# Kernel optimization log

Hardware: AMD Instinct MI355X
Metric: run time of the kernel (lower is better)

## Reference

```python
import jax, jax.numpy as jnp
import numpy as np

NG = 8       # GroupNorm groups
EPS = 1e-5   # torch default eps for GroupNorm/BatchNorm
M_AND = 5    # Anderson history size
MAX_ITER = 25
LAM = 1e-4
BETA = 1.0


def conv2d(x, w):
    # x: [B,C,H,W], w: [O,I,3,3], stride 1, SAME padding (pad=1)
    return jax.lax.conv_general_dilated(x, w, (1, 1), 'SAME',
                                        dimension_numbers=('NCHW', 'OIHW', 'NCHW'))


def group_norm(x, g, b):
    B, C, H, W = x.shape
    xg = x.reshape(B, NG, C // NG, H, W)
    mu = xg.mean((2, 3, 4), keepdims=True)
    var = xg.var((2, 3, 4), keepdims=True)
    xn = ((xg - mu) * jax.lax.rsqrt(var + EPS)).reshape(B, C, H, W)
    return xn * g[None, :, None, None] + b[None, :, None, None]


def batch_norm(x, g, b):
    # training-mode BatchNorm2d: batch statistics over (B,H,W)
    mu = x.mean((0, 2, 3), keepdims=True)
    var = x.var((0, 2, 3), keepdims=True)
    return (x - mu) * jax.lax.rsqrt(var + EPS) * g[None, :, None, None] + b[None, :, None, None]


def resnet_f(p, z, x):
    # y = norm1(relu(conv1(z))); out = norm3(relu(z + norm2(x + conv2(y))))
    y = group_norm(jax.nn.relu(conv2d(z, p['conv1_w'])), p['gn1_g'], p['gn1_b'])
    return group_norm(jax.nn.relu(z + group_norm(x + conv2d(y, p['conv2_w']),
                                                 p['gn2_g'], p['gn2_b'])),
                      p['gn3_g'], p['gn3_b'])


def anderson(f, x0, m=M_AND, lam=LAM, max_iter=MAX_ITER, beta=BETA):
    # Anderson acceleration for fixed point z = f(z); fixed iteration count
    # (the torch version early-exits at tol=0.01; we run the full max_iter for
    # a deterministic jit-friendly reference).
    shape = x0.shape
    bsz = shape[0]
    flat = lambda v: v.reshape(bsz, -1)
    X = [None] * m
    Fv = [None] * m
    X[0] = flat(x0)
    Fv[0] = flat(f(x0))
    X[1] = Fv[0]
    Fv[1] = flat(f(Fv[0].reshape(shape)))
    for k in range(2, max_iter):
        n = min(k, m)
        Xn = jnp.stack(X[:n], 1)   # [B,n,D]
        Fn = jnp.stack(Fv[:n], 1)  # [B,n,D]
        G = Fn - Xn
        Hm = jnp.einsum('bnd,bmd->bnm', G, G) + lam * jnp.eye(n, dtype=x0.dtype)
        Hb = (jnp.zeros((bsz, n + 1, n + 1), x0.dtype)
              .at[:, 1:, 1:].set(Hm)
              .at[:, 0, 1:].set(1.0)
              .at[:, 1:, 0].set(1.0))
        y = jnp.zeros((bsz, n + 1), x0.dtype).at[:, 0].set(1.0)
        alpha = jnp.linalg.solve(Hb, y[..., None])[:, 1:, 0]  # [B,n]
        xk = beta * jnp.einsum('bn,bnd->bd', alpha, Fn) + (1.0 - beta) * jnp.einsum('bn,bnd->bd', alpha, Xn)
        X[k % m] = xk
        Fv[k % m] = flat(f(xk.reshape(shape)))
    return X[(max_iter - 1) % m].reshape(shape)


def setup_inputs() -> dict:
    key = jax.random.key(0)
    ks = jax.random.split(key, 6)
    B, H, W = 8, 128, 200
    f32 = jnp.float32
    return {
        'x': jax.random.normal(ks[0], (B, 1, H, W), f32),
        'conv0_w': jax.random.normal(ks[1], (48, 1, 3, 3), f32) * 0.1,
        'conv0_b': jnp.zeros((48,), f32),
        'bn_g': jnp.ones((48,), f32),
        'bn_b': jnp.zeros((48,), f32),
        'conv1_w': jax.random.normal(ks[2], (64, 48, 3, 3), f32) * 0.01,
        'conv2_w': jax.random.normal(ks[3], (48, 64, 3, 3), f32) * 0.01,
        'gn1_g': jnp.ones((64,), f32), 'gn1_b': jnp.zeros((64,), f32),
        'gn2_g': jnp.ones((48,), f32), 'gn2_b': jnp.zeros((48,), f32),
        'gn3_g': jnp.ones((48,), f32), 'gn3_b': jnp.zeros((48,), f32),
        'fc_w': jax.random.normal(ks[4], (10, 200), f32) * 0.05,
        'fc_b': jnp.zeros((10,), f32),
    }


def reference(x, conv0_w, conv0_b, bn_g, bn_b, conv1_w, conv2_w,
              gn1_g, gn1_b, gn2_g, gn2_b, gn3_g, gn3_b, fc_w, fc_b):
    fp = {'conv1_w': conv1_w, 'conv2_w': conv2_w,
          'gn1_g': gn1_g, 'gn1_b': gn1_b,
          'gn2_g': gn2_g, 'gn2_b': gn2_b,
          'gn3_g': gn3_g, 'gn3_b': gn3_b}
    h = batch_norm(conv2d(x, conv0_w) + conv0_b[None, :, None, None], bn_g, bn_b)
    z_star = anderson(lambda z: resnet_f(fp, z, h), jnp.zeros_like(h))
    z = resnet_f(fp, z_star, h)  # one extra application, as in DEQFixedPoint
    # Linear(200,10) acts on last dim: [B,48,H,200] -> [B,48,H,10]
    return jnp.einsum('bchw,ow->bcho', z, fc_w) + fc_b
```

## Files before the change

### kernel.cpp

```cpp
#include <hip/hip_runtime.h>

#define BB   8
#define HH   128
#define WW   200
#define HWSZ 25600
#define C48  48
#define C64  64
#define NGRP 8
#define EPSV 1e-5f
#define LAMV 1e-4
#define SLOT 9830400
#define DPB  1228800
#define Y64SZ 13107200
#define BIGELEMS 131072000ull

typedef unsigned short bf16_t;
typedef __attribute__((ext_vector_type(4))) short s4v;
typedef __attribute__((ext_vector_type(8))) short s8v;
typedef __attribute__((ext_vector_type(16))) float f32x16;

__device__ inline float b2f(bf16_t b) { return __uint_as_float(((unsigned)b) << 16); }
__device__ inline bf16_t f2b(float f) {
    unsigned u = __float_as_uint(f);
    unsigned r = u + 0x7fffu + ((u >> 16) & 1u);
    return (bf16_t)(r >> 16);
}
__device__ inline float lo16(unsigned u) { return __uint_as_float(u << 16); }
__device__ inline float hi16(unsigned u) { return __uint_as_float(u & 0xffff0000u); }
__device__ inline unsigned pack2(float lo, float hi) {
    return ((unsigned)f2b(lo)) | (((unsigned)f2b(hi)) << 16);
}
__device__ inline float4 ld4(const bf16_t* p) {
    ushort4 u = *(const ushort4*)p;
    return make_float4(b2f(u.x), b2f(u.y), b2f(u.z), b2f(u.w));
}
__device__ inline void st4(bf16_t* p, float4 v) {
    ushort4 u; u.x = f2b(v.x); u.y = f2b(v.y); u.z = f2b(v.z); u.w = f2b(v.w);
    *(ushort4*)p = u;
}
__device__ inline void ld8(const bf16_t* p, float* v) {
    uint4 u = *(const uint4*)p;
    v[0] = lo16(u.x); v[1] = hi16(u.x); v[2] = lo16(u.y); v[3] = hi16(u.y);
    v[4] = lo16(u.z); v[5] = hi16(u.z); v[6] = lo16(u.w); v[7] = hi16(u.w);
}
__device__ inline void st8(bf16_t* p, const float* v) {
    uint4 u;
    u.x = pack2(v[0], v[1]); u.y = pack2(v[2], v[3]);
    u.z = pack2(v[4], v[5]); u.w = pack2(v[6], v[7]);
    *(uint4*)p = u;
}

__device__ inline void ms_from(const double* __restrict__ ds, int pair, double invcnt,
                               float& mean, float& inv) {
    double s = ds[2 * pair], q = ds[2 * pair + 1];
    double m = s * invcnt;
    double v = q * invcnt - m * m;
    mean = (float)m;
    inv = (float)(1.0 / sqrt(v + (double)EPSV));
}


__global__ void zero_kernel(float* __restrict__ p, int n) {
    int i = blockIdx.x * 256 + threadIdx.x;
    if (i < n) p[i] = 0.f;
}
__global__ void fill16_kernel(float4* __restrict__ p) {
    float4 z; z.x = z.y = z.z = z.w = 0.f;
    p[(size_t)blockIdx.x * 256 + threadIdx.x] = z;
}
__global__ void copy16_kernel(float4* __restrict__ dst, const float4* __restrict__ src) {
    size_t i = (size_t)blockIdx.x * 256 + threadIdx.x;
    dst[i] = src[i];
}

__global__ void pack_kernel(const float* __restrict__ w, bf16_t* __restrict__ apk,
                            int CIN, int CO_real, int total) {
    int idx = blockIdx.x * 256 + threadIdx.x;
    if (idx >= total) return;
    int j   = idx & 7;
    int l   = (idx >> 3) & 63;
    int mt  = (idx >> 9) & 1;
    int tap = (idx >> 10) % 9;
    int kc  = idx / 9216;
    int co = mt * 32 + (l & 31);
    int ci = kc * 16 + (l >> 5) * 8 + j;
    float v = (co < CO_real) ? w[((size_t)co * CIN + ci) * 9 + tap] : 0.f;
    apk[idx] = f2b(v);
}

__global__ __launch_bounds__(256) void conv0_kernel(
    const float* __restrict__ x, const float* __restrict__ w0,
    const float* __restrict__ b0, float* __restrict__ out)
{
    __shared__ float xs[3 * 202];
    __shared__ float wt[480];
    const int tid = threadIdx.x;
    const int bI = blockIdx.x / HH, y = blockIdx.x % HH;
    for (int i = tid; i < 606; i += 256) {
        int r = i / 202, cc = i % 202;
        int gy = y + r - 1, gx = cc - 1;
        float v = 0.f;
        if ((unsigned)gy < (unsigned)HH && (unsigned)gx < (unsigned)WW)
            v = x[(size_t)bI * HWSZ + gy * WW + gx];
        xs[r * 202 + cc] = v;
    }
    for (int i = tid; i < 480; i += 256) wt[i] = (i < 432) ? w0[i] : b0[i - 432];
    __syncthreads();
    const size_t obase = (((size_t)bI * HH + y) * WW) * 48;
    for (int ch = tid; ch < 2400; ch += 256) {
        int px = (ch * 4) / 48, c0 = (ch * 4) % 48;
        float xv[3][3];
        #pragma unroll
        for (int r = 0; r < 3; r++)
            #pragma unroll
            for (int dx = 0; dx < 3; dx++)
                xv[r][dx] = xs[r * 202 + px + dx];
        float4 o;
        #pragma unroll
        for (int j = 0; j < 4; j++) {
            int c = c0 + j;
            float acc = wt[432 + c];
            #pragma unroll
            for (int r = 0; r < 3; r++)
                #pragma unroll
                for (int dx = 0; dx < 3; dx++)
                    acc = fmaf(xv[r][dx], wt[c * 9 + r * 3 + dx], acc);
            ((float*)&o)[j] = acc;
        }
        *(float4*)(out + obase + ch * 4) = o;
    }
}

__global__ void bn_stats_kernel(const float* __restrict__ src, double* __restrict__ dst)
{
    __shared__ float ss[192], qq[192];
    const int tid = threadIdx.x;
    const int c = tid % 48, r = tid / 48;
    const int b = blockIdx.y;
    const size_t base = ((size_t)b * HWSZ + (size_t)blockIdx.x * 256) * 48 + c;
    float s = 0.f, q = 0.f;
    for (int p = r; p < 256; p += 4) {
        float v = src[base + (size_t)p * 48];
        s += v; q += v * v;
    }
    ss[tid] = s; qq[tid] = q;
    __syncthreads();
    if (tid < 48) {
        s = ss[tid] + ss[tid + 48] + ss[tid + 96] + ss[tid + 144];
        q = qq[tid] + qq[tid + 48] + qq[tid + 96] + qq[tid + 144];
        unsafeAtomicAdd(&dst[tid * 2],     (double)s);
        unsafeAtomicAdd(&dst[tid * 2 + 1], (double)q);
    }
}

__global__ __launch_bounds__(256) void bn_apply_kernel(
    const float* __restrict__ src, bf16_t* __restrict__ dst,
    const float* __restrict__ gamma, const float* __restrict__ beta,
    const double* __restrict__ ds)
{
    __shared__ float gaT[48], beT[48];
    int tid = threadIdx.x;
    if (tid < 48) {
        float mean, inv; ms_from(ds, tid, 1.0 / 204800.0, mean, inv);
        float ga = gamma[tid] * inv;
        gaT[tid] = ga; beT[tid] = beta[tid] - mean * ga;
    }
    __syncthreads();
    size_t base = (size_t)blockIdx.x * 1024 + (size_t)tid * 4;
    int c0 = (int)(base % 48);
    float4 v = *(const float4*)(src + base);
    ushort4 o;
    o.x = f2b(fmaf(v.x, gaT[c0],     beT[c0]));
    o.y = f2b(fmaf(v.y, gaT[c0 + 1], beT[c0 + 1]));
    o.z = f2b(fmaf(v.z, gaT[c0 + 2], beT[c0 + 2]));
    o.w = f2b(fmaf(v.w, gaT[c0 + 3], beT[c0 + 3]));
    *(ushort4*)(dst + base) = o;
}

template<int CIN, int CIPAD, int CO, int OTS, int CG, bool RELU, bool ADDH, bool FOLDGN>
__global__ __launch_bounds__(512) void conv_mfma_kernel(
    const bf16_t* __restrict__ in, const s8v* __restrict__ apk,
    const bf16_t* __restrict__ hadd, bf16_t* __restrict__ out,
    double* __restrict__ dsOut,
    const double* __restrict__ dsPrev, const float* __restrict__ gPrev,
    const float* __restrict__ bPrev)
{
    constexpr int KC  = CIN / 16;
    constexpr int NCH = CIN / 4;
    const int tid  = threadIdx.x;
    const int lane = tid & 63;
    const int wv   = tid >> 6;
    const int x0 = blockIdx.x * 32;
    const int y0 = blockIdx.y * 8;
    const int b  = blockIdx.z;

    __shared__ __align__(16) bf16_t bt[10 * 34 * CIPAD];
    __shared__ __align__(16) float gaT[FOLDGN ? CIN : 4];
    __shared__ __align__(16) float beT[FOLDGN ? CIN : 4];
    __shared__ float ss[512], qq[512];

    if (FOLDGN) {
        if (tid < CIN) {
            float mean, inv;
            ms_from(dsPrev, b * NGRP + tid / (CIN / NGRP), 1.0 / 204800.0, mean, inv);
            float ga = gPrev[tid] * inv;
            gaT[tid] = ga; beT[tid] = bPrev[tid] - mean * ga;
        }
        __syncthreads();
    }
    for (int i = tid; i < 10 * 34 * NCH; i += 512) {
        int ch = i % NCH, p = i / NCH;
        int r = p / 34, c = p - r * 34;
        int gy = y0 + r - 1, gx = x0 + c - 1;
        ushort4 v = make_ushort4(0, 0, 0, 0);
        if ((unsigned)gy < (unsigned)HH && (unsigned)gx < (unsigned)WW) {
            ushort4 raw = *(const ushort4*)(in + ((((size_t)b * HH + gy) * WW + gx) * CIN + ch * 4));
            if (FOLDGN) {
                float4 ga4 = *(const float4*)&gaT[ch * 4];
                float4 be4 = *(const float4*)&beT[ch * 4];
                v.x = f2b(fmaf(b2f(raw.x), ga4.x, be4.x));
                v.y = f2b(fmaf(b2f(raw.y), ga4.y, be4.y));
                v.z = f2b(fmaf(b2f(raw.z), ga4.z, be4.z));
                v.w = f2b(fmaf(b2f(raw.w), ga4.w, be4.w));
            } else v = raw;
        }
        *(ushort4*)(bt + p * CIPAD + ch * 4) = v;
    }
    __syncthreads();

    const int n = lane & 31, half = lane >> 5;
    f32x16 acc0, acc1;
    #pragma unroll
    for (int i = 0; i < 16; i++) { acc0[i] = 0.f; acc1[i] = 0.f; }

    #pragma unroll
    for (int ky = 0; ky < 3; ky++)
    #pragma unroll
    for (int kx = 0; kx < 3; kx++) {
        const int tap = ky * 3 + kx;
        s8v af[2 * KC];
        #pragma unroll
        for (int kc = 0; kc < KC; kc++) {
            af[2 * kc]     = apk[(size_t)kc * 1152 + tap * 128 + lane];
            af[2 * kc + 1] = apk[(size_t)kc * 1152 + tap * 128 + 64 + lane];
        }
        const bf16_t* brow = bt + ((wv + ky) * 34 + n + kx) * CIPAD + half * 8;
        #pragma unroll
        for (int kc = 0; kc < KC; kc++) {
            s8v bfrag = *(const s8v*)(brow + kc * 16);
            acc0 = __builtin_amdgcn_mfma_f32_32x32x16_bf16(af[2 * kc],     bfrag, acc0, 0, 0, 0);
            acc1 = __builtin_amdgcn_mfma_f32_32x32x16_bf16(af[2 * kc + 1], bfrag, acc1, 0, 0, 0);
        }
    }
    __syncthreads();

    bf16_t* ot = bt;
    {
        const int pxl = wv * 32 + n;
        const bool pv = (x0 + n) < WW;
        #pragma unroll
        for (int g4 = 0; g4 < 4; g4++) {
            s4v pk0;
            #pragma unroll
            for (int jj = 0; jj < 4; jj++) {
                float v = acc0[g4 * 4 + jj];
                if (RELU) v = fmaxf(v, 0.f);
                pk0[jj] = (short)(pv ? f2b(v) : (bf16_t)0);
            }
            *(s4v*)&ot[pxl * OTS + g4 * 8 + 4 * half] = pk0;
            const int c1b = 32 + g4 * 8 + 4 * half;
            if (c1b + 3 < CO) {
                s4v pk1;
                #pragma unroll
                for (int jj = 0; jj < 4; jj++) {
                    float v = acc1[g4 * 4 + jj];
                    if (RELU) v = fmaxf(v, 0.f);
                    pk1[jj] = (short)(pv ? f2b(v) : (bf16_t)0);
                }
                *(s4v*)&ot[pxl * OTS + c1b] = pk1;
            }
        }
    }
    __syncthreads();
    {
        constexpr int NCH8 = 256 * CO / 8;
        for (int ch = tid; ch < NCH8; ch += 512) {
            int pxl = ch / (CO / 8);
            int co0 = (ch % (CO / 8)) * 8;
            int row = pxl >> 5, col = pxl & 31;
            int xx = x0 + col;
            if (xx < WW) {
                bf16_t* lp = &ot[pxl * OTS + co0];
                size_t ga = (((size_t)b * HH + y0 + row) * WW + xx) * CO + co0;
                if (ADDH) {
                    float4 h0 = ld4(hadd + ga), h1 = ld4(hadd + ga + 4);
                    float4 l0 = ld4(lp), l1 = ld4(lp + 4);
                    float4 v0 = make_float4(l0.x + h0.x, l0.y + h0.y, l0.z + h0.z, l0.w + h0.w);
                    float4 v1 = make_float4(l1.x + h1.x, l1.y + h1.y, l1.z + h1.z, l1.w + h1.w);
                    st4(out + ga, v0); st4(out + ga + 4, v1);
                    st4(lp, v0); st4(lp + 4, v1);
                } else {
                    *(ushort4*)(out + ga)     = *(ushort4*)lp;
                    *(ushort4*)(out + ga + 4) = *(ushort4*)(lp + 4);
                }
            }
        }
    }
    if (ADDH) __syncthreads();
    {
        constexpr int NPH = 512 / CO;
        const int c = tid % CO, rr = tid / CO;
        float s = 0.f, q = 0.f;
        if (rr < NPH) {
            for (int px = rr; px < 256; px += NPH) {
                float v = b2f(ot[px * OTS + c]);
                s += v; q += v * v;
            }
        }
        ss[tid] = s; qq[tid] = q;
        __syncthreads();
        if (tid < CO) {
            float S = ss[tid], Q = qq[tid];
            #pragma unroll
            for (int p = 1; p < NPH; p++) { S += ss[tid + p * CO]; Q += qq[tid + p * CO]; }
            ss[tid] = S; qq[tid] = Q;
        }
        __syncthreads();
        if (tid < NGRP) {
            float S = 0.f, Q = 0.f;
            #pragma unroll
            for (int j = 0; j < CG; j++) { S += ss[tid * CG + j]; Q += qq[tid * CG + j]; }
            unsafeAtomicAdd(&dsOut[((size_t)b * NGRP + tid) * 2],     (double)S);
            unsafeAtomicAdd(&dsOut[((size_t)b * NGRP + tid) * 2 + 1], (double)Q);
        }
    }
}

__global__ __launch_bounds__(192) void add_relu_gn2_kernel(
    bf16_t* __restrict__ u, const bf16_t* __restrict__ z,
    const double* __restrict__ ds2, const float* __restrict__ g2,
    const float* __restrict__ b2, double* __restrict__ ds3)
{
    __shared__ float sm[16];
    const int tid = threadIdx.x;
    const int c0 = 8 * (tid % 6), pxr = tid / 6;
    const int b = blockIdx.y;
    if (tid < 16) sm[tid] = 0.f;
    const int gA = c0 / 6;
    const int split = (gA + 1) * 6 - c0;
    float meanA, invA, meanB, invB;
    ms_from(ds2, b * NGRP + gA,     1.0 / 153600.0, meanA, invA);
    ms_from(ds2, b * NGRP + gA + 1, 1.0 / 153600.0, meanB, invB);
    float wga[8], wbe[8];
    #pragma unroll
    for (int e = 0; e < 8; e++) {
        int c = c0 + e;
        float m = (e < split) ? meanA : meanB, iv = (e < split) ? invA : invB;
        float ga = g2[c] * iv;
        wga[e] = ga; wbe[e] = b2[c] - m * ga;
    }
    __syncthreads();
    const size_t pxbase = (size_t)b * HWSZ + (size_t)blockIdx.x * 256;
    float sA = 0.f, qA = 0.f, sB = 0.f, qB = 0.f;
    for (int it = 0; it < 8; it++) {
        size_t idx = (pxbase + it * 32 + pxr) * 48 + c0;
        float uu[8], zz[8], vv[8];
        ld8(u + idx, uu); ld8(z + idx, zz);
        #pragma unroll
        for (int e = 0; e < 8; e++) {
            float v = fmaxf(fmaf(uu[e], wga[e], wbe[e]) + zz[e], 0.f);
            vv[e] = v;
            if (e < split) { sA += v; qA += v * v; } else { sB += v; qB += v * v; }
        }
        st8(u + idx, vv);
    }
    atomicAdd(&sm[2 * gA], sA);     atomicAdd(&sm[2 * gA + 1], qA);
    atomicAdd(&sm[2 * gA + 2], sB); atomicAdd(&sm[2 * gA + 3], qB);
    __syncthreads();
    if (tid < NGRP) {
        unsafeAtomicAdd(&ds3[(b * NGRP + tid) * 2],     (double)sm[tid * 2]);
        unsafeAtomicAdd(&ds3[(b * NGRP + tid) * 2 + 1], (double)sm[tid * 2 + 1]);
    }
}

__global__ __launch_bounds__(192) void gn3_gram_kernel(
    const bf16_t* __restrict__ v, const bf16_t* __restrict__ z,
    bf16_t* __restrict__ F, bf16_t* __restrict__ G,
    const double* __restrict__ ds3, const float* __restrict__ g3,
    const float* __restrict__ b3,
    const bf16_t* __restrict__ Gall, int jslot, int nf, double* __restrict__ gram)
{
    __shared__ double red[3][5];
    const int tid = threadIdx.x;
    const int c0 = 8 * (tid % 6), pxr = tid / 6;
    const int b = blockIdx.y;
    const int gA = c0 / 6;
    const int split = (gA + 1) * 6 - c0;
    float meanA, invA, meanB, invB;
    ms_from(ds3, b * NGRP + gA,     1.0 / 153600.0, meanA, invA);
    ms_from(ds3, b * NGRP + gA + 1, 1.0 / 153600.0, meanB, invB);
    float wga[8], wbe[8];
    #pragma unroll
    for (int e = 0; e < 8; e++) {
        int c = c0 + e;
        float m = (e < split) ? meanA : meanB, iv = (e < split) ? invA : invB;
        float ga = g3[c] * iv;
        wga[e] = ga; wbe[e] = b3[c] - m * ga;
    }
    const size_t pxbase = (size_t)b * HWSZ + (size_t)blockIdx.x * 256;
    double dot[5] = {0.0, 0.0, 0.0, 0.0, 0.0};
    for (int it = 0; it < 8; it++) {
        size_t idx = (pxbase + it * 32 + pxr) * 48 + c0;
        float rr[8];
        ld8(v + idx, rr);
        #pragma unroll
        for (int e = 0; e < 8; e++) rr[e] = fmaf(rr[e], wga[e], wbe[e]);
        st8(F + idx, rr);
        if (nf > 0) {
            float zz[8], gg[8];
            ld8(z + idx, zz);
            #pragma unroll
            for (int e = 0; e < 8; e++) gg[e] = rr[e] - zz[e];
            st8(G + idx, gg);
            #pragma unroll
            for (int i = 0; i < 5; i++) {
                if (i >= nf) continue;
                float d = 0.f;
                if (i == jslot) {
                    #pragma unroll
                    for (int e = 0; e < 8; e++) d = fmaf(gg[e], gg[e], d);
                } else {
                    float gi[8];
                    ld8(Gall + (size_t)i * SLOT + idx, gi);
                    #pragma unroll
                    for (int e = 0; e < 8; e++) d = fmaf(gg[e], gi[e], d);
                }
                dot[i] += (double)d;
            }
        }
    }
    if (nf > 0) {
        #pragma unroll
        for (int i = 0; i < 5; i++) {
            if (i >= nf) continue;
            #pragma unroll
            for (int off = 32; off > 0; off >>= 1) dot[i] += __shfl_down(dot[i], off);
        }
        int wv = tid >> 6;
        if ((tid & 63) == 0) {
            #pragma unroll
            for (int i = 0; i < 5; i++) if (i < nf) red[wv][i] = dot[i];
        }
        __syncthreads();
        if (tid == 0) {
            #pragma unroll
            for (int i = 0; i < 5; i++) {
                if (i >= nf) continue;
                double D = red[0][i] + red[1][i] + red[2][i];
                unsafeAtomicAdd(&gram[b * 25 + jslot * 5 + i], D);
                if (i != jslot) unsafeAtomicAdd(&gram[b * 25 + i * 5 + jslot], D);
            }
        }
    }
}


__global__ void solve_kernel(const double* __restrict__ gram, float* __restrict__ alpha, int n) {
    int b = threadIdx.x;
    if (b >= BB) return;
    const int m = n + 1;
    double A[6][7];
    for (int i = 0; i < m; i++)
        for (int jj = 0; jj <= m; jj++) A[i][jj] = 0.0;
    for (int i = 1; i < m; i++) { A[0][i] = 1.0; A[i][0] = 1.0; }
    for (int i = 1; i < m; i++)
        for (int jj = 1; jj < m; jj++)
            A[i][jj] = gram[b * 25 + (i - 1) * 5 + (jj - 1)] + ((i == jj) ? LAMV : 0.0);
    A[0][m] = 1.0;
    for (int col = 0; col < m; col++) {
        int piv = col; double best = fabs(A[col][col]);
        for (int rr = col + 1; rr < m; rr++) {
            double tv = fabs(A[rr][col]);
            if (tv > best) { best = tv; piv = rr; }
        }
        if (piv != col)
            for (int cc = col; cc <= m; cc++) {
                double tmp = A[col][cc]; A[col][cc] = A[piv][cc]; A[piv][cc] = tmp;
            }
        double invp = 1.0 / A[col][col];
        for (int cc = col; cc <= m; cc++) A[col][cc] *= invp;
        for (int rr = 0; rr < m; rr++) {
            if (rr == col) continue;
            double f = A[rr][col];
            if (f != 0.0)
                for (int cc = col; cc <= m; cc++) A[rr][cc] = fma(-f, A[col][cc], A[rr][cc]);
        }
    }
    for (int i = 0; i < n; i++) alpha[b * 5 + i] = (float)A[i + 1][m];
}

__global__ __launch_bounds__(256) void xk_kernel(
    const bf16_t* __restrict__ Fb, const float* __restrict__ alpha,
    bf16_t* __restrict__ zcur, int n, double* __restrict__ gram, int jz, int nf)
{
    if (blockIdx.x == 0 && threadIdx.x < 8 * nf) {
        int b = threadIdx.x / nf, i = threadIdx.x % nf;
        gram[b * 25 + jz * 5 + i] = 0.0;
        gram[b * 25 + i * 5 + jz] = 0.0;
    }
    const int b = blockIdx.x / 75;
    float al[5];
    #pragma unroll
    for (int j = 0; j < 5; j++) al[j] = (j < n) ? alpha[b * 5 + j] : 0.f;
    const size_t base = (size_t)blockIdx.x * 16384 + (size_t)threadIdx.x * 8;
    for (int it = 0; it < 8; it++) {
        size_t idx = base + (size_t)it * 2048;
        float s[8] = {0.f, 0.f, 0.f, 0.f, 0.f, 0.f, 0.f, 0.f};
        #pragma unroll
        for (int j = 0; j < 5; j++) {
            if (j < n) {
                float f[8];
                ld8(Fb + (size_t)j * SLOT + idx, f);
                #pragma unroll
                for (int e = 0; e < 8; e++) s[e] = fmaf(f[e], al[j], s[e]);
            }
        }
        st8(zcur + idx, s);
    }
}

__global__ __launch_bounds__(512) void fc_kernel(
    const bf16_t* __restrict__ zf, const float* __restrict__ fw,
    const float* __restrict__ fb, float* __restrict__ out)
{
    __shared__ bf16_t row[9600];
    __shared__ float fwT[2000];
    int tid = threadIdx.x;
    int b = blockIdx.x >> 7, hh = blockIdx.x & 127;
    size_t base = (((size_t)b * HH + hh) * WW) * 48;
    for (int i = tid; i < 2400; i += 512)
        *(ushort4*)&row[i * 4] = *(const ushort4*)(zf + base + (size_t)i * 4);
    for (int i = tid; i < 2000; i += 512) fwT[i] = fw[i];
    __syncthreads();
    if (tid < 480) {
        int c = tid % 48, o = tid / 48;
        float acc = fb[o];
        #pragma unroll 4
        for (int w = 0; w < 200; w++)
            acc = fmaf(b2f(row[w * 48 + c]), fwT[o * 200 + w], acc);
        out[(((size_t)b * 48 + c) * HH + hh) * 10 + o] = acc;
    }
}


static inline int imin(int a, int b) { return a < b ? a : b; }

extern "C" void kernel_launch(void* const* d_in, const int* in_sizes, int n_in,
                              void* d_out, int out_size, void* d_ws, size_t ws_size,
                              hipStream_t stream)
{
    const float* x   = (const float*)d_in[0];
    const float* w0  = (const float*)d_in[1];
    const float* b0  = (const float*)d_in[2];
    const float* bng = (const float*)d_in[3];
    const float* bnb = (const float*)d_in[4];
    const float* w1  = (const float*)d_in[5];
    const float* w2  = (const float*)d_in[6];
    const float* g1  = (const float*)d_in[7];
    const float* be1 = (const float*)d_in[8];
    const float* g2  = (const float*)d_in[9];
    const float* be2 = (const float*)d_in[10];
    const float* g3  = (const float*)d_in[11];
    const float* be3 = (const float*)d_in[12];
    const float* fcw = (const float*)d_in[13];
    const float* fcb = (const float*)d_in[14];
    float* out = (float*)d_out;

    bf16_t* h    = (bf16_t*)d_ws;
    bf16_t* zcur = h + (size_t)SLOT;
    bf16_t* y64  = zcur + (size_t)SLOT;
    bf16_t* Fb   = y64 + (size_t)Y64SZ;
    bf16_t* Gb   = Fb + 5 * (size_t)SLOT;
    double* dstats = (double*)((char*)d_ws + BIGELEMS * 2);
    double* gram   = dstats + 9696;
    float*  alpha  = (float*)(gram + 200);
    bf16_t* apk1   = (bf16_t*)(alpha + 40);
    bf16_t* apk2   = apk1 + 27648;
    float*  scratch = (float*)Gb;

    const size_t need = BIGELEMS * 2 + 9696 * 8 + 200 * 8 + 40 * 4 + (27648 + 36864) * 2;
    if (ws_size < need) return;

    const dim3 blk(256);
    const int CHUNKS16 = SLOT * 2 / 16 / 256;

    zero_kernel<<<(19792 + 255) / 256, blk, 0, stream>>>((float*)dstats, 19792);
    pack_kernel<<<108, blk, 0, stream>>>(w1, apk1, 48, 64, 27648);
    pack_kernel<<<144, blk, 0, stream>>>(w2, apk2, 64, 48, 36864);
    fill16_kernel<<<CHUNKS16, blk, 0, stream>>>((float4*)zcur);

    conv0_kernel<<<BB * HH, blk, 0, stream>>>(x, w0, b0, scratch);
    bn_stats_kernel<<<dim3(100, BB), dim3(192), 0, stream>>>(scratch, dstats);
    bn_apply_kernel<<<SLOT / 1024, blk, 0, stream>>>(scratch, h, bng, bnb, dstats);

    int call = 0;
    auto resnet = [&](const bf16_t* zin, bf16_t* Fdst, bf16_t* Gdst, int jslot, int nf) {
        double* ds = dstats + 96 + 384 * call;
        call++;
        dim3 cg(7, 16, BB);
        conv_mfma_kernel<48, 56, 64, 66, 8, true, false, false><<<cg, dim3(512), 0, stream>>>(
            zin, (const s8v*)apk1, nullptr, y64, ds, nullptr, nullptr, nullptr);
        conv_mfma_kernel<64, 72, 48, 50, 6, false, true, true><<<cg, dim3(512), 0, stream>>>(
            y64, (const s8v*)apk2, h, Fdst, ds + 128, ds, g1, be1);
        add_relu_gn2_kernel<<<dim3(100, BB), dim3(192), 0, stream>>>(
            Fdst, zin, ds + 128, g2, be2, ds + 256);
        gn3_gram_kernel<<<dim3(100, BB), dim3(192), 0, stream>>>(
            Fdst, zin, Fdst, Gdst, ds + 256, g3, be3, Gb, jslot, nf, gram);
    };

    resnet(zcur, Fb, Gb, 0, 1);
    copy16_kernel<<<CHUNKS16, blk, 0, stream>>>((float4*)zcur, (const float4*)Fb);
    resnet(zcur, Fb + (size_t)SLOT, Gb + (size_t)SLOT, 1, 2);

    for (int k = 2; k <= 24; k++) {
        int n = imin(k, 5);
        int j = k % 5;
        int nf = imin(k + 1, 5);
        solve_kernel<<<1, 64, 0, stream>>>(gram, alpha, n);
        xk_kernel<<<600, blk, 0, stream>>>(Fb, alpha, zcur, n, gram, j, nf);
        if (k < 24)
            resnet(zcur, Fb + (size_t)j * SLOT, Gb + (size_t)j * SLOT, j, nf);
    }

    resnet(zcur, Fb, nullptr, 0, 0);

    fc_kernel<<<BB * HH, dim3(512), 0, stream>>>(Fb, fcw, fcb, out);
}
```

Measured before the change: 4.970 ms.

## Shrink conv tiles, double-buffer weight loads, fuse Anderson solve into xk

The MFMA conv kernel moves from 512-thread blocks over 8 rows to 256-thread blocks over 4 rows with launch bounds (256,4). This aims for more resident blocks per CU and finer-grained scheduling, at the cost of more halo reloads. Weight fragment loads are now double-buffered across taps so global loads overlap the MFMAs. The separate solve kernel is dropped: each xk block redundantly solves the small Anderson system in one thread, and the gram zeroing moves into add_relu_gn2, removing one launch per iteration.

```diff
diff --git a/kernel.cpp b/kernel.cpp
--- a/kernel.cpp
+++ b/kernel.cpp
@@ -178,7 +178,7 @@
 }
 
 template<int CIN, int CIPAD, int CO, int OTS, int CG, bool RELU, bool ADDH, bool FOLDGN>
-__global__ __launch_bounds__(512) void conv_mfma_kernel(
+__global__ __launch_bounds__(256, 4) void conv_mfma_kernel(
     const bf16_t* __restrict__ in, const s8v* __restrict__ apk,
     const bf16_t* __restrict__ hadd, bf16_t* __restrict__ out,
     double* __restrict__ dsOut,
@@ -191,13 +191,13 @@
     const int lane = tid & 63;
     const int wv   = tid >> 6;
     const int x0 = blockIdx.x * 32;
-    const int y0 = blockIdx.y * 8;
+    const int y0 = blockIdx.y * 4;
     const int b  = blockIdx.z;
 
-    __shared__ __align__(16) bf16_t bt[10 * 34 * CIPAD];
+    __shared__ __align__(16) bf16_t bt[6 * 34 * CIPAD];
     __shared__ __align__(16) float gaT[FOLDGN ? CIN : 4];
     __shared__ __align__(16) float beT[FOLDGN ? CIN : 4];
-    __shared__ float ss[512], qq[512];
+    __shared__ float ss[256], qq[256];
 
     if (FOLDGN) {
         if (tid < CIN) {
@@ -208,7 +208,7 @@
         }
         __syncthreads();
     }
-    for (int i = tid; i < 10 * 34 * NCH; i += 512) {
+    for (int i = tid; i < 6 * 34 * NCH; i += 256) {
         int ch = i % NCH, p = i / NCH;
         int r = p / 34, c = p - r * 34;
         int gy = y0 + r - 1, gx = x0 + c - 1;
@@ -233,25 +233,36 @@
     #pragma unroll
     for (int i = 0; i < 16; i++) { acc0[i] = 0.f; acc1[i] = 0.f; }
 
-    #pragma unroll
-    for (int ky = 0; ky < 3; ky++)
-    #pragma unroll
-    for (int kx = 0; kx < 3; kx++) {
-        const int tap = ky * 3 + kx;
-        s8v af[2 * KC];
+    const s8v* apw = apk + lane;
+    s8v afA[2 * KC], afB[2 * KC];
+
+    auto ld_tap = [&](int tap, s8v* dst) {
         #pragma unroll
         for (int kc = 0; kc < KC; kc++) {
-            af[2 * kc]     = apk[(size_t)kc * 1152 + tap * 128 + lane];
-            af[2 * kc + 1] = apk[(size_t)kc * 1152 + tap * 128 + 64 + lane];
-        }
+            dst[2 * kc]     = apw[(size_t)kc * 1152 + tap * 128];
+            dst[2 * kc + 1] = apw[(size_t)kc * 1152 + tap * 128 + 64];
+        }
+    };
+    auto do_tap = [&](int tap, const s8v* cur) {
+        const int ky = tap / 3, kx = tap % 3;
         const bf16_t* brow = bt + ((wv + ky) * 34 + n + kx) * CIPAD + half * 8;
         #pragma unroll
         for (int kc = 0; kc < KC; kc++) {
             s8v bfrag = *(const s8v*)(brow + kc * 16);
-            acc0 = __builtin_amdgcn_mfma_f32_32x32x16_bf16(af[2 * kc],     bfrag, acc0, 0, 0, 0);
-            acc1 = __builtin_amdgcn_mfma_f32_32x32x16_bf16(af[2 * kc + 1], bfrag, acc1, 0, 0, 0);
-        }
-    }
+            acc0 = __builtin_amdgcn_mfma_f32_32x32x16_bf16(cur[2 * kc],     bfrag, acc0, 0, 0, 0);
+            acc1 = __builtin_amdgcn_mfma_f32_32x32x16_bf16(cur[2 * kc + 1], bfrag, acc1, 0, 0, 0);
+        }
+    };
+
+    ld_tap(0, afA);
+    #pragma unroll
+    for (int t = 0; t < 4; t++) {
+        ld_tap(2 * t + 1, afB);
+        do_tap(2 * t, afA);
+        if (2 * t + 2 < 9) ld_tap(2 * t + 2, afA);
+        do_tap(2 * t + 1, afB);
+    }
+    do_tap(8, afA);
     __syncthreads();
 
     bf16_t* ot = bt;
@@ -283,8 +294,8 @@
     }
     __syncthreads();
     {
-        constexpr int NCH8 = 256 * CO / 8;
-        for (int ch = tid; ch < NCH8; ch += 512) {
+        constexpr int NCH8 = 128 * CO / 8;
+        for (int ch = tid; ch < NCH8; ch += 256) {
             int pxl = ch / (CO / 8);
             int co0 = (ch % (CO / 8)) * 8;
             int row = pxl >> 5, col = pxl & 31;
@@ -308,11 +319,11 @@
     }
     if (ADDH) __syncthreads();
     {
-        constexpr int NPH = 512 / CO;
+        constexpr int NPH = 256 / CO;
         const int c = tid % CO, rr = tid / CO;
         float s = 0.f, q = 0.f;
         if (rr < NPH) {
-            for (int px = rr; px < 256; px += NPH) {
+            for (int px = rr; px < 128; px += NPH) {
                 float v = b2f(ot[px * OTS + c]);
                 s += v; q += v * v;
             }
@@ -339,10 +350,16 @@
 __global__ __launch_bounds__(192) void add_relu_gn2_kernel(
     bf16_t* __restrict__ u, const bf16_t* __restrict__ z,
     const double* __restrict__ ds2, const float* __restrict__ g2,
-    const float* __restrict__ b2, double* __restrict__ ds3)
+    const float* __restrict__ b2, double* __restrict__ ds3,
+    double* __restrict__ gram, int jz, int nfz)
 {
     __shared__ float sm[16];
     const int tid = threadIdx.x;
+    if (blockIdx.x == 0 && blockIdx.y == 0 && tid < 8 * nfz) {
+        int bb = tid / nfz, i = tid % nfz;
+        gram[bb * 25 + jz * 5 + i] = 0.0;
+        gram[bb * 25 + i * 5 + jz] = 0.0;
+    }
     const int c0 = 8 * (tid % 6), pxr = tid / 6;
     const int b = blockIdx.y;
     if (tid < 16) sm[tid] = 0.f;
@@ -464,54 +481,48 @@
     }
 }
 
-
-__global__ void solve_kernel(const double* __restrict__ gram, float* __restrict__ alpha, int n) {
-    int b = threadIdx.x;
-    if (b >= BB) return;
-    const int m = n + 1;
-    double A[6][7];
-    for (int i = 0; i < m; i++)
-        for (int jj = 0; jj <= m; jj++) A[i][jj] = 0.0;
-    for (int i = 1; i < m; i++) { A[0][i] = 1.0; A[i][0] = 1.0; }
-    for (int i = 1; i < m; i++)
-        for (int jj = 1; jj < m; jj++)
-            A[i][jj] = gram[b * 25 + (i - 1) * 5 + (jj - 1)] + ((i == jj) ? LAMV : 0.0);
-    A[0][m] = 1.0;
-    for (int col = 0; col < m; col++) {
-        int piv = col; double best = fabs(A[col][col]);
-        for (int rr = col + 1; rr < m; rr++) {
-            double tv = fabs(A[rr][col]);
-            if (tv > best) { best = tv; piv = rr; }
-        }
-        if (piv != col)
-            for (int cc = col; cc <= m; cc++) {
-                double tmp = A[col][cc]; A[col][cc] = A[piv][cc]; A[piv][cc] = tmp;
-            }
-        double invp = 1.0 / A[col][col];
-        for (int cc = col; cc <= m; cc++) A[col][cc] *= invp;
-        for (int rr = 0; rr < m; rr++) {
-            if (rr == col) continue;
-            double f = A[rr][col];
-            if (f != 0.0)
-                for (int cc = col; cc <= m; cc++) A[rr][cc] = fma(-f, A[col][cc], A[rr][cc]);
-        }
-    }
-    for (int i = 0; i < n; i++) alpha[b * 5 + i] = (float)A[i + 1][m];
-}
-
 __global__ __launch_bounds__(256) void xk_kernel(
-    const bf16_t* __restrict__ Fb, const float* __restrict__ alpha,
-    bf16_t* __restrict__ zcur, int n, double* __restrict__ gram, int jz, int nf)
-{
-    if (blockIdx.x == 0 && threadIdx.x < 8 * nf) {
-        int b = threadIdx.x / nf, i = threadIdx.x % nf;
-        gram[b * 25 + jz * 5 + i] = 0.0;
-        gram[b * 25 + i * 5 + jz] = 0.0;
-    }
+    const bf16_t* __restrict__ Fb, const double* __restrict__ gram,
+    bf16_t* __restrict__ zcur, int n)
+{
+    __shared__ float alf[5];
     const int b = blockIdx.x / 75;
+    if (threadIdx.x == 0) {
+        const int m = n + 1;
+        double A[6][7];
+        for (int i = 0; i < m; i++)
+            for (int jj = 0; jj <= m; jj++) A[i][jj] = 0.0;
+        for (int i = 1; i < m; i++) { A[0][i] = 1.0; A[i][0] = 1.0; }
+        for (int i = 1; i < m; i++)
+            for (int jj = 1; jj < m; jj++)
+                A[i][jj] = gram[b * 25 + (i - 1) * 5 + (jj - 1)] + ((i == jj) ? LAMV : 0.0);
+        A[0][m] = 1.0;
+        for (int col = 0; col < m; col++) {
+            int piv = col; double best = fabs(A[col][col]);
+            for (int rr = col + 1; rr < m; rr++) {
+                double tv = fabs(A[rr][col]);
+                if (tv > best) { best = tv; piv = rr; }
+            }
+            if (piv != col)
+                for (int cc = col; cc <= m; cc++) {
+                    double tmp = A[col][cc]; A[col][cc] = A[piv][cc]; A[piv][cc] = tmp;
+                }
+            double invp = 1.0 / A[col][col];
+            for (int cc = col; cc <= m; cc++) A[col][cc] *= invp;
+            for (int rr = 0; rr < m; rr++) {
+                if (rr == col) continue;
+                double f = A[rr][col];
+                if (f != 0.0)
+                    for (int cc = col; cc <= m; cc++) A[rr][cc] = fma(-f, A[col][cc], A[rr][cc]);
+            }
+        }
+        #pragma unroll
+        for (int i = 0; i < 5; i++) alf[i] = (i < n) ? (float)A[i + 1][m] : 0.f;
+    }
+    __syncthreads();
     float al[5];
     #pragma unroll
-    for (int j = 0; j < 5; j++) al[j] = (j < n) ? alpha[b * 5 + j] : 0.f;
+    for (int j = 0; j < 5; j++) al[j] = alf[j];
     const size_t base = (size_t)blockIdx.x * 16384 + (size_t)threadIdx.x * 8;
     for (int it = 0; it < 8; it++) {
         size_t idx = base + (size_t)it * 2048;
@@ -607,13 +618,13 @@
     auto resnet = [&](const bf16_t* zin, bf16_t* Fdst, bf16_t* Gdst, int jslot, int nf) {
         double* ds = dstats + 96 + 384 * call;
         call++;
-        dim3 cg(7, 16, BB);
-        conv_mfma_kernel<48, 56, 64, 66, 8, true, false, false><<<cg, dim3(512), 0, stream>>>(
+        dim3 cg(7, 32, BB);
+        conv_mfma_kernel<48, 56, 64, 66, 8, true, false, false><<<cg, dim3(256), 0, stream>>>(
             zin, (const s8v*)apk1, nullptr, y64, ds, nullptr, nullptr, nullptr);
-        conv_mfma_kernel<64, 72, 48, 50, 6, false, true, true><<<cg, dim3(512), 0, stream>>>(
+        conv_mfma_kernel<64, 72, 48, 50, 6, false, true, true><<<cg, dim3(256), 0, stream>>>(
             y64, (const s8v*)apk2, h, Fdst, ds + 128, ds, g1, be1);
         add_relu_gn2_kernel<<<dim3(100, BB), dim3(192), 0, stream>>>(
-            Fdst, zin, ds + 128, g2, be2, ds + 256);
+            Fdst, zin, ds + 128, g2, be2, ds + 256, gram, jslot, nf);
         gn3_gram_kernel<<<dim3(100, BB), dim3(192), 0, stream>>>(
             Fdst, zin, Fdst, Gdst, ds + 256, g3, be3, Gb, jslot, nf, gram);
     };
@@ -626,8 +637,7 @@
         int n = imin(k, 5);
         int j = k % 5;
         int nf = imin(k + 1, 5);
-        solve_kernel<<<1, 64, 0, stream>>>(gram, alpha, n);
-        xk_kernel<<<600, blk, 0, stream>>>(Fb, alpha, zcur, n, gram, j, nf);
+        xk_kernel<<<600, blk, 0, stream>>>(Fb, gram, zcur, n);
         if (k < 24)
             resnet(zcur, Fb + (size_t)j * SLOT, Gb + (size_t)j * SLOT, j, nf);
     }
```

After: 5.539 ms. +11.5%, slower.
